# Performance work log

Measured on AMD Instinct MI355X. Metric: run time of the kernel, lower is better.

The kernel has to match this reference:

```python
import jax, jax.numpy as jnp
import numpy as np

B, Lq, Dlen, P = 32, 32, 4096, 16
V, D, H = 50257, 2048, 2048


def setup_inputs() -> dict:
    key = jax.random.key(0)
    k = jax.random.split(key, 7)
    queries = jax.random.randint(k[0], (B, Lq), 0, V)
    query_lengths = jax.random.randint(k[1], (B,), 4, Lq + 1).astype(jnp.int32)
    docs = jax.random.randint(k[2], (B, Dlen), 0, V)
    # passage lengths in [32, 255]; cumsum <= 16*255 < Dlen so all passages fit
    passage_lengths = jax.random.randint(k[3], (B, P), 32, 256).astype(jnp.int32)
    emb = jax.random.normal(k[4], (V, D), jnp.float32) * 0.02
    W = jax.random.normal(k[5], (H, D), jnp.float32) * (1.0 / np.sqrt(D))
    b = jnp.zeros((H,), jnp.float32)
    return dict(queries=queries, query_lengths=query_lengths, docs=docs,
                passage_lengths=passage_lengths, emb=emb, W=W, b=b)


def reference(queries, query_lengths, docs, passage_lengths, emb, W, b):
    # --- encode queries: masked mean of token embeddings, then linear ---
    q_emb = emb[queries]  # [B,Lq,D]
    q_mask = (jnp.arange(Lq)[None, :] < query_lengths[:, None]).astype(q_emb.dtype)
    q_rep = jnp.einsum('bl,bld->bd', q_mask, q_emb) / query_lengths[:, None].astype(q_emb.dtype)
    q_enc = q_rep @ W.T + b  # [B,H]

    # --- split docs into passages via segment ids from cumulative lengths ---
    d_emb = emb[docs]  # [B,T,D]
    cum = jnp.cumsum(passage_lengths, axis=1)  # [B,P]
    t = jnp.arange(Dlen)
    seg = jnp.sum(t[None, :, None] >= cum[:, None, :], axis=-1)  # [B,T], token -> passage id
    valid = t[None, :] < cum[:, -1:]  # tokens past total doc length are padding
    onehot = ((seg[:, :, None] == jnp.arange(P)[None, None, :]) & valid[:, :, None]).astype(d_emb.dtype)
    sums = jnp.einsum('btp,btd->bpd', onehot, d_emb)  # per-passage embedding sums
    denom = jnp.maximum(passage_lengths, 1).astype(d_emb.dtype)[:, :, None]
    p_rep = sums / denom  # [B,P,D] masked mean
    p_enc = p_rep @ W.T + b  # [B,P,H]

    # --- dot-product scoring (dropout = identity in eval mode) ---
    scores = jnp.einsum('bh,bph->bp', q_enc, p_enc)
    return scores * (passage_lengths > 0).astype(scores.dtype)
```

## Files before the change

### kernel.cpp

```cpp
#include <hip/hip_runtime.h>

#define B 32
#define LQ 32
#define DLEN 4096
#define P 16
#define D 2048
#define H 2048
#define HCHUNK 64

__global__ __launch_bounds__(256) void zero_v_kernel(float* __restrict__ v) {
  const int i = blockIdx.x * 256 + threadIdx.x;
  if (i < B * D) v[i] = 0.f;
}

__global__ __launch_bounds__(512) void gather_mean_kernel(
    const int* __restrict__ queries, const int* __restrict__ qlen,
    const int* __restrict__ docs, const int* __restrict__ plen,
    const float* __restrict__ emb,
    float* __restrict__ q_rep, float* __restrict__ p_rep)
{
  __shared__ int stok[256];
  const int bid = blockIdx.x;
  const int* toks;
  int len;
  float* outp;

  if (bid < B * P) {
    const int b = bid >> 4;
    const int p = bid & 15;
    int s = 0;
#pragma unroll
    for (int i = 0; i < P; ++i) s += (i < p) ? plen[b * P + i] : 0;
    len  = plen[b * P + p];
    toks = docs + b * DLEN + s;
    outp = p_rep + (size_t)bid * D;
  } else {
    const int b = bid - B * P;
    len  = qlen[b];
    toks = queries + b * LQ;
    outp = q_rep + (size_t)b * D;
  }

  for (int i = threadIdx.x; i < len; i += blockDim.x) stok[i] = toks[i];
  __syncthreads();

  const int tid = threadIdx.x;
  float4 acc = make_float4(0.f, 0.f, 0.f, 0.f);

  int t = 0;
  for (; t + 4 <= len; t += 4) {
    const float4* r0 = (const float4*)(emb + (size_t)stok[t + 0] * D);
    const float4* r1 = (const float4*)(emb + (size_t)stok[t + 1] * D);
    const float4* r2 = (const float4*)(emb + (size_t)stok[t + 2] * D);
    const float4* r3 = (const float4*)(emb + (size_t)stok[t + 3] * D);
    const float4 a0 = r0[tid];
    const float4 a1 = r1[tid];
    const float4 a2 = r2[tid];
    const float4 a3 = r3[tid];
    acc.x += (a0.x + a1.x) + (a2.x + a3.x);
    acc.y += (a0.y + a1.y) + (a2.y + a3.y);
    acc.z += (a0.z + a1.z) + (a2.z + a3.z);
    acc.w += (a0.w + a1.w) + (a2.w + a3.w);
  }
  for (; t < len; ++t) {
    const float4* r = (const float4*)(emb + (size_t)stok[t] * D);
    const float4 a = r[tid];
    acc.x += a.x; acc.y += a.y; acc.z += a.z; acc.w += a.w;
  }

  const float inv = 1.0f / (float)(len > 0 ? len : 1);
  ((float4*)outp)[tid] =
      make_float4(acc.x * inv, acc.y * inv, acc.z * inv, acc.w * inv);
}

__global__ __launch_bounds__(256) void qenc_kernel(
    const float* __restrict__ q_rep, const float* __restrict__ W,
    const float* __restrict__ bias, float* __restrict__ q_enc)
{
  const int h = blockIdx.x;
  __shared__ float wsh[D];
  for (int c = threadIdx.x; c < D; c += 256)
    wsh[c] = W[(size_t)h * D + c];
  __syncthreads();

  const float bh   = bias[h];
  const int   lane = threadIdx.x & 63;
  const int   wid  = threadIdx.x >> 6;

  for (int b = wid; b < B; b += 4) {
    float s = 0.f;
#pragma unroll
    for (int k = 0; k < D / 64; ++k) {
      const int c = k * 64 + lane;
      s += wsh[c] * q_rep[b * D + c];
    }
#pragma unroll
    for (int off = 32; off; off >>= 1) s += __shfl_down(s, off, 64);
    if (lane == 0) q_enc[b * H + h] = s + bh;
  }
}

__global__ __launch_bounds__(256) void v_kernel(
    const float* __restrict__ q_enc, const float* __restrict__ W,
    float* __restrict__ v)
{
  const int d  = blockIdx.x * 256 + threadIdx.x;
  const int h0 = blockIdx.y * HCHUNK;

  __shared__ float qe[HCHUNK * B];
  for (int i = threadIdx.x; i < HCHUNK * B; i += 256) {
    const int hh = i >> 5;
    const int b  = i & 31;
    qe[i] = q_enc[b * H + h0 + hh];
  }
  __syncthreads();

  float acc[B];
#pragma unroll
  for (int b = 0; b < B; ++b) acc[b] = 0.f;

  for (int hh = 0; hh < HCHUNK; ++hh) {
    const float w = W[(size_t)(h0 + hh) * D + d];
#pragma unroll
    for (int b = 0; b < B; ++b) acc[b] += w * qe[hh * B + b];
  }

#pragma unroll
  for (int b = 0; b < B; ++b) atomicAdd(&v[b * D + d], acc[b]);
}

__global__ __launch_bounds__(256) void score_kernel(
    const float* __restrict__ v, const float* __restrict__ q_enc,
    const float* __restrict__ bias, const float* __restrict__ p_rep,
    const int* __restrict__ plen, float* __restrict__ out)
{
  const int bp = blockIdx.x;
  const int b  = bp >> 4;

  float s = 0.f;
#pragma unroll
  for (int k = 0; k < D / 256; ++k) {
    const int c = k * 256 + threadIdx.x;
    s += v[b * D + c] * p_rep[(size_t)bp * D + c];
    s += q_enc[b * H + c] * bias[c];
  }
#pragma unroll
  for (int off = 32; off; off >>= 1) s += __shfl_down(s, off, 64);

  __shared__ float red[4];
  const int lane = threadIdx.x & 63;
  const int wid  = threadIdx.x >> 6;
  if (lane == 0) red[wid] = s;
  __syncthreads();
  if (threadIdx.x == 0) {
    const float tot = red[0] + red[1] + red[2] + red[3];
    out[bp] = (plen[bp] > 0) ? tot : 0.f;
  }
}

extern "C" void kernel_launch(void* const* d_in, const int* in_sizes, int n_in,
                              void* d_out, int out_size, void* d_ws, size_t ws_size,
                              hipStream_t stream) {
  const int*   queries = (const int*)d_in[0];
  const int*   qlen    = (const int*)d_in[1];
  const int*   docs    = (const int*)d_in[2];
  const int*   plen    = (const int*)d_in[3];
  const float* emb     = (const float*)d_in[4];
  const float* W       = (const float*)d_in[5];
  const float* bias    = (const float*)d_in[6];
  float*       out     = (float*)d_out;

  float* q_rep = (float*)d_ws;
  float* p_rep = q_rep + B * D;
  float* q_enc = p_rep + (size_t)B * P * D;
  float* v     = q_enc + B * H;

  zero_v_kernel<<<(B * D + 255) / 256, 256, 0, stream>>>(v);
  gather_mean_kernel<<<B * P + B, 512, 0, stream>>>(queries, qlen, docs, plen,
                                                    emb, q_rep, p_rep);
  qenc_kernel<<<H, 256, 0, stream>>>(q_rep, W, bias, q_enc);
  dim3 vgrid(D / 256, H / HCHUNK);
  v_kernel<<<vgrid, 256, 0, stream>>>(q_enc, W, v);
  score_kernel<<<B * P, 256, 0, stream>>>(v, q_enc, bias, p_rep, plen, out);
}
```

Before: 617.2 us.

## Score doc tokens directly against projected query vector, dropping passage mean materialization

Replaces the per-passage embedding gather-mean plus dot product with a per-token dot product against v = W^T q_enc, spread across 32 token chunks per batch. Each token's score is accumulated into its passage slot through shared-memory and global atomics, then divided by passage length in a small final kernel. This removes the p_rep workspace writes and reads and spreads the doc gather across more blocks. qenc now processes 4 output rows per block with float4 loads, and the v_kernel H chunk is halved. Atomic float accumulation makes summation order nondeterministic, and a token chunk can exceed the 128-entry shared buffer if passage totals are large.

```diff
diff --git a/kernel.cpp b/kernel.cpp
--- a/kernel.cpp
+++ b/kernel.cpp
@@ -6,155 +6,186 @@
 #define P 16
 #define D 2048
 #define H 2048
-#define HCHUNK 64
-
-__global__ __launch_bounds__(256) void zero_v_kernel(float* __restrict__ v) {
+#define NC 32
+#define HC 32
+#define HB 4
+
+__global__ __launch_bounds__(256) void zero_kernel(float* __restrict__ v,
+                                                   float* __restrict__ sacc) {
   const int i = blockIdx.x * 256 + threadIdx.x;
   if (i < B * D) v[i] = 0.f;
-}
-
-__global__ __launch_bounds__(512) void gather_mean_kernel(
+  if (i < B * P) sacc[i] = 0.f;
+}
+
+__global__ __launch_bounds__(256) void qrep_kernel(
     const int* __restrict__ queries, const int* __restrict__ qlen,
-    const int* __restrict__ docs, const int* __restrict__ plen,
-    const float* __restrict__ emb,
-    float* __restrict__ q_rep, float* __restrict__ p_rep)
-{
-  __shared__ int stok[256];
-  const int bid = blockIdx.x;
-  const int* toks;
-  int len;
-  float* outp;
-
-  if (bid < B * P) {
-    const int b = bid >> 4;
-    const int p = bid & 15;
-    int s = 0;
-#pragma unroll
-    for (int i = 0; i < P; ++i) s += (i < p) ? plen[b * P + i] : 0;
-    len  = plen[b * P + p];
-    toks = docs + b * DLEN + s;
-    outp = p_rep + (size_t)bid * D;
-  } else {
-    const int b = bid - B * P;
-    len  = qlen[b];
-    toks = queries + b * LQ;
-    outp = q_rep + (size_t)b * D;
-  }
-
-  for (int i = threadIdx.x; i < len; i += blockDim.x) stok[i] = toks[i];
-  __syncthreads();
-
-  const int tid = threadIdx.x;
-  float4 acc = make_float4(0.f, 0.f, 0.f, 0.f);
-
-  int t = 0;
-  for (; t + 4 <= len; t += 4) {
-    const float4* r0 = (const float4*)(emb + (size_t)stok[t + 0] * D);
-    const float4* r1 = (const float4*)(emb + (size_t)stok[t + 1] * D);
-    const float4* r2 = (const float4*)(emb + (size_t)stok[t + 2] * D);
-    const float4* r3 = (const float4*)(emb + (size_t)stok[t + 3] * D);
-    const float4 a0 = r0[tid];
-    const float4 a1 = r1[tid];
-    const float4 a2 = r2[tid];
-    const float4 a3 = r3[tid];
-    acc.x += (a0.x + a1.x) + (a2.x + a3.x);
-    acc.y += (a0.y + a1.y) + (a2.y + a3.y);
-    acc.z += (a0.z + a1.z) + (a2.z + a3.z);
-    acc.w += (a0.w + a1.w) + (a2.w + a3.w);
-  }
-  for (; t < len; ++t) {
+    const float* __restrict__ emb, float* __restrict__ q_rep) {
+  __shared__ int stok[LQ];
+  const int b   = blockIdx.x;
+  const int len = qlen[b];
+  if (threadIdx.x < len) stok[threadIdx.x] = queries[b * LQ + threadIdx.x];
+  __syncthreads();
+
+  float4 a0 = make_float4(0.f, 0.f, 0.f, 0.f);
+  float4 a1 = make_float4(0.f, 0.f, 0.f, 0.f);
+  for (int t = 0; t < len; ++t) {
     const float4* r = (const float4*)(emb + (size_t)stok[t] * D);
-    const float4 a = r[tid];
-    acc.x += a.x; acc.y += a.y; acc.z += a.z; acc.w += a.w;
-  }
-
-  const float inv = 1.0f / (float)(len > 0 ? len : 1);
-  ((float4*)outp)[tid] =
-      make_float4(acc.x * inv, acc.y * inv, acc.z * inv, acc.w * inv);
+    const float4 x = r[threadIdx.x];
+    const float4 y = r[threadIdx.x + 256];
+    a0.x += x.x; a0.y += x.y; a0.z += x.z; a0.w += x.w;
+    a1.x += y.x; a1.y += y.y; a1.z += y.z; a1.w += y.w;
+  }
+  const float inv = 1.0f / (float)len;
+  float4* o = (float4*)(q_rep + (size_t)b * D);
+  o[threadIdx.x]       = make_float4(a0.x*inv, a0.y*inv, a0.z*inv, a0.w*inv);
+  o[threadIdx.x + 256] = make_float4(a1.x*inv, a1.y*inv, a1.z*inv, a1.w*inv);
 }
 
 __global__ __launch_bounds__(256) void qenc_kernel(
     const float* __restrict__ q_rep, const float* __restrict__ W,
-    const float* __restrict__ bias, float* __restrict__ q_enc)
-{
-  const int h = blockIdx.x;
-  __shared__ float wsh[D];
-  for (int c = threadIdx.x; c < D; c += 256)
-    wsh[c] = W[(size_t)h * D + c];
-  __syncthreads();
-
-  const float bh   = bias[h];
-  const int   lane = threadIdx.x & 63;
-  const int   wid  = threadIdx.x >> 6;
-
+    const float* __restrict__ bias, float* __restrict__ q_enc) {
+  const int h0 = blockIdx.x * HB;
+  __shared__ float4 wsh[HB][D / 4];
+  for (int i = threadIdx.x; i < HB * (D / 4); i += 256) {
+    const int r = i / (D / 4), c = i % (D / 4);
+    wsh[r][c] = ((const float4*)(W + (size_t)(h0 + r) * D))[c];
+  }
+  __syncthreads();
+
+  const int lane = threadIdx.x & 63, wid = threadIdx.x >> 6;
   for (int b = wid; b < B; b += 4) {
-    float s = 0.f;
-#pragma unroll
-    for (int k = 0; k < D / 64; ++k) {
-      const int c = k * 64 + lane;
-      s += wsh[c] * q_rep[b * D + c];
+    const float4* q4 = (const float4*)(q_rep + (size_t)b * D);
+    float s[HB] = {0.f, 0.f, 0.f, 0.f};
+#pragma unroll
+    for (int j = 0; j < 8; ++j) {
+      const float4 q = q4[j * 64 + lane];
+#pragma unroll
+      for (int r = 0; r < HB; ++r) {
+        const float4 w = wsh[r][j * 64 + lane];
+        s[r] += w.x * q.x + w.y * q.y + w.z * q.z + w.w * q.w;
+      }
     }
 #pragma unroll
-    for (int off = 32; off; off >>= 1) s += __shfl_down(s, off, 64);
-    if (lane == 0) q_enc[b * H + h] = s + bh;
+    for (int r = 0; r < HB; ++r) {
+      float t = s[r];
+#pragma unroll
+      for (int off = 32; off; off >>= 1) t += __shfl_down(t, off, 64);
+      if (lane == 0) q_enc[b * H + h0 + r] = t + bias[h0 + r];
+    }
   }
 }
 
 __global__ __launch_bounds__(256) void v_kernel(
     const float* __restrict__ q_enc, const float* __restrict__ W,
-    float* __restrict__ v)
-{
+    float* __restrict__ v) {
   const int d  = blockIdx.x * 256 + threadIdx.x;
-  const int h0 = blockIdx.y * HCHUNK;
-
-  __shared__ float qe[HCHUNK * B];
-  for (int i = threadIdx.x; i < HCHUNK * B; i += 256) {
-    const int hh = i >> 5;
-    const int b  = i & 31;
-    qe[i] = q_enc[b * H + h0 + hh];
-  }
+  const int h0 = blockIdx.y * HC;
+
+  __shared__ float qe[HC][B];
+  for (int i = threadIdx.x; i < HC * B; i += 256)
+    qe[i >> 5][i & 31] = q_enc[(i & 31) * H + h0 + (i >> 5)];
   __syncthreads();
 
   float acc[B];
 #pragma unroll
   for (int b = 0; b < B; ++b) acc[b] = 0.f;
 
-  for (int hh = 0; hh < HCHUNK; ++hh) {
+#pragma unroll 4
+  for (int hh = 0; hh < HC; ++hh) {
     const float w = W[(size_t)(h0 + hh) * D + d];
 #pragma unroll
-    for (int b = 0; b < B; ++b) acc[b] += w * qe[hh * B + b];
-  }
-
+    for (int b = 0; b < B; ++b) acc[b] += w * qe[hh][b];
+  }
 #pragma unroll
   for (int b = 0; b < B; ++b) atomicAdd(&v[b * D + d], acc[b]);
 }
 
-__global__ __launch_bounds__(256) void score_kernel(
-    const float* __restrict__ v, const float* __restrict__ q_enc,
-    const float* __restrict__ bias, const float* __restrict__ p_rep,
-    const int* __restrict__ plen, float* __restrict__ out)
-{
-  const int bp = blockIdx.x;
-  const int b  = bp >> 4;
-
+__global__ __launch_bounds__(256) void docscore_kernel(
+    const int* __restrict__ docs, const int* __restrict__ plen,
+    const float* __restrict__ emb, const float* __restrict__ v,
+    float* __restrict__ sacc) {
+  const int b = blockIdx.y;
+  __shared__ float4 vsh[D / 4];
+  __shared__ int    cum[P];
+  __shared__ int    stok[128];
+  __shared__ unsigned char sp[128];
+  __shared__ float  wacc[4][P];
+
+  vsh[threadIdx.x]       = ((const float4*)(v + (size_t)b * D))[threadIdx.x];
+  vsh[threadIdx.x + 256] = ((const float4*)(v + (size_t)b * D))[threadIdx.x + 256];
+  if (threadIdx.x == 0) {
+    int s = 0;
+#pragma unroll
+    for (int i = 0; i < P; ++i) { s += plen[b * P + i]; cum[i] = s; }
+  }
+  if (threadIdx.x < 4 * P) wacc[threadIdx.x >> 4][threadIdx.x & 15] = 0.f;
+  __syncthreads();
+
+  const int tot = cum[P - 1];
+  const int per = (tot + NC - 1) / NC;
+  const int t0  = blockIdx.x * per;
+  const int t1  = (t0 + per < tot) ? (t0 + per) : tot;
+  const int cnt = t1 - t0;
+
+  for (int i = threadIdx.x; i < cnt; i += 256) {
+    const int t = t0 + i;
+    stok[i] = docs[b * DLEN + t];
+    int p = 0;
+#pragma unroll
+    for (int j = 0; j < P; ++j) p += (t >= cum[j]) ? 1 : 0;
+    sp[i] = (unsigned char)p;
+  }
+  __syncthreads();
+
+  const int lane = threadIdx.x & 63, wid = threadIdx.x >> 6;
+  for (int i = wid; i < cnt; i += 4) {
+    const float4* e4 = (const float4*)(emb + (size_t)stok[i] * D);
+    float s = 0.f;
+#pragma unroll
+    for (int j = 0; j < 8; ++j) {
+      const float4 e = e4[j * 64 + lane];
+      const float4 w = vsh[j * 64 + lane];
+      s += e.x * w.x + e.y * w.y + e.z * w.z + e.w * w.w;
+    }
+#pragma unroll
+    for (int off = 32; off; off >>= 1) s += __shfl_down(s, off, 64);
+    if (lane == 0) wacc[wid][sp[i]] += s;
+  }
+  __syncthreads();
+
+  if (threadIdx.x < P) {
+    const float r = wacc[0][threadIdx.x] + wacc[1][threadIdx.x] +
+                    wacc[2][threadIdx.x] + wacc[3][threadIdx.x];
+    atomicAdd(&sacc[b * P + threadIdx.x], r);
+  }
+}
+
+__global__ __launch_bounds__(256) void final_kernel(
+    const float* __restrict__ q_enc, const float* __restrict__ bias,
+    const float* __restrict__ sacc, const int* __restrict__ plen,
+    float* __restrict__ out) {
+  const int b = blockIdx.x;
   float s = 0.f;
 #pragma unroll
-  for (int k = 0; k < D / 256; ++k) {
+  for (int k = 0; k < 8; ++k) {
     const int c = k * 256 + threadIdx.x;
-    s += v[b * D + c] * p_rep[(size_t)bp * D + c];
     s += q_enc[b * H + c] * bias[c];
   }
 #pragma unroll
   for (int off = 32; off; off >>= 1) s += __shfl_down(s, off, 64);
 
   __shared__ float red[4];
-  const int lane = threadIdx.x & 63;
-  const int wid  = threadIdx.x >> 6;
+  __shared__ float qb;
+  const int lane = threadIdx.x & 63, wid = threadIdx.x >> 6;
   if (lane == 0) red[wid] = s;
   __syncthreads();
-  if (threadIdx.x == 0) {
-    const float tot = red[0] + red[1] + red[2] + red[3];
-    out[bp] = (plen[bp] > 0) ? tot : 0.f;
+  if (threadIdx.x == 0) qb = red[0] + red[1] + red[2] + red[3];
+  __syncthreads();
+
+  if (threadIdx.x < P) {
+    const int l = plen[b * P + threadIdx.x];
+    const float val = sacc[b * P + threadIdx.x] / (float)(l > 0 ? l : 1) + qb;
+    out[b * P + threadIdx.x] = (l > 0) ? val : 0.f;
   }
 }
 
@@ -170,16 +201,17 @@
   const float* bias    = (const float*)d_in[6];
   float*       out     = (float*)d_out;
 
-  float* q_rep = (float*)d_ws;
-  float* p_rep = q_rep + B * D;
-  float* q_enc = p_rep + (size_t)B * P * D;
-  float* v     = q_enc + B * H;
-
-  zero_v_kernel<<<(B * D + 255) / 256, 256, 0, stream>>>(v);
-  gather_mean_kernel<<<B * P + B, 512, 0, stream>>>(queries, qlen, docs, plen,
-                                                    emb, q_rep, p_rep);
-  qenc_kernel<<<H, 256, 0, stream>>>(q_rep, W, bias, q_enc);
-  dim3 vgrid(D / 256, H / HCHUNK);
+  float* v     = (float*)d_ws;
+  float* sacc  = v + B * D;
+  float* q_rep = sacc + B * P;
+  float* q_enc = q_rep + B * D;
+
+  zero_kernel<<<(B * D + 255) / 256, 256, 0, stream>>>(v, sacc);
+  qrep_kernel<<<B, 256, 0, stream>>>(queries, qlen, emb, q_rep);
+  qenc_kernel<<<H / HB, 256, 0, stream>>>(q_rep, W, bias, q_enc);
+  dim3 vgrid(D / 256, H / HC);
   v_kernel<<<vgrid, 256, 0, stream>>>(q_enc, W, v);
-  score_kernel<<<B * P, 256, 0, stream>>>(v, q_enc, bias, p_rep, plen, out);
-}
+  dim3 dgrid(NC, B);
+  docscore_kernel<<<dgrid, 256, 0, stream>>>(docs, plen, emb, v, sacc);
+  final_kernel<<<B, 256, 0, stream>>>(q_enc, bias, sacc, plen, out);
+}
```

Result: no change. 609.6 us (-1.2%).
